# Kernel optimization log

Hardware: AMD Instinct MI355X
Metric: run time of the kernel (lower is better)

## Reference

```python
import jax, jax.numpy as jnp
import numpy as np

N_TYPES = 4
AEV_DIM = 384
HIDDEN = [160, 128, 96]
CELU_ALPHA = 0.1


def _init_params(key):
    dims = [AEV_DIM] + HIDDEN + [1]
    params = {}
    for li in range(len(dims) - 1):
        key, kw = jax.random.split(key)
        scale = 1.0 / np.sqrt(dims[li])
        # stacked over the N_TYPES per-atom-type experts
        params[f"W{li}"] = (jax.random.normal(kw, (N_TYPES, dims[li], dims[li + 1]), dtype=jnp.float32) * scale)
        params[f"b{li}"] = jnp.zeros((N_TYPES, dims[li + 1]), dtype=jnp.float32)
    return params


def setup_inputs() -> dict:
    key = jax.random.key(0)
    k1, k2, k3 = jax.random.split(key, 3)
    B, A = 2048, 64
    species = jax.random.randint(k1, (B, A), 0, N_TYPES, dtype=jnp.int64)
    aev = jax.random.normal(k2, (B, A, AEV_DIM), dtype=jnp.float32)
    inp = {"species": species, "aev": aev}
    inp.update(_init_params(k3))
    return inp


def _mlp(x, t, W0, b0, W1, b1, W2, b2, W3, b3):
    # x: [N, aev_dim] -> [N] per-atom energy for atom type t
    h = jax.nn.celu(x @ W0[t] + b0[t], alpha=CELU_ALPHA)
    h = jax.nn.celu(h @ W1[t] + b1[t], alpha=CELU_ALPHA)
    h = jax.nn.celu(h @ W2[t] + b2[t], alpha=CELU_ALPHA)
    return (h @ W3[t] + b3[t]).reshape(-1)


def reference(species, aev, W0, b0, W1, b1, W2, b2, W3, b3):
    B, A = species.shape
    sp = species.reshape(-1)            # [B*A]
    x = aev.reshape(-1, aev.shape[-1])  # [B*A, aev_dim]
    out = jnp.zeros(sp.shape, dtype=aev.dtype)  # padding_fill = 0
    for t in range(N_TYPES):  # fixed small expert set
        y = _mlp(x, t, W0, b0, W1, b1, W2, b2, W3, b3)
        out = jnp.where(sp == t, y, out)
    energies = out.reshape(B, A).sum(axis=1)  # reduce over atoms
    return species, energies
```

## Files before the change

### kernel.cpp

```cpp
#include <hip/hip_runtime.h>
#include <hip/hip_bf16.h>
#include <math.h>


#define NATOMS   131072
#define NMOL     2048
#define AEV      384
#define NTYPES   4
#define MBLK     64
#define PADTOT   (NATOMS + NTYPES * MBLK)
#define NBLK_MLP (PADTOT / MBLK)
#define NBLK_H   512

#define WB_L1 61440
#define WB_L2 81920
#define WB_T  94208

typedef __attribute__((ext_vector_type(8))) short bf16x8;
typedef __attribute__((ext_vector_type(4))) float f32x4;

__device__ __forceinline__ float celu01(float v) {
  return (v > 0.f) ? v : 0.1f * (__expf(v * 10.f) - 1.f);
}
__device__ __forceinline__ unsigned short f2bf(float x) {
  unsigned u = __float_as_uint(x);
  return (unsigned short)((u + 0x7FFFu + ((u >> 16) & 1u)) >> 16);
}
__device__ __forceinline__ unsigned int pk2(float lo, float hi) {
  union { __hip_bfloat162 h; unsigned int u; } c;
  c.h = __float22bfloat162_rn(make_float2(lo, hi));
  return c.u;
}
__device__ __forceinline__ bf16x8 cvt8(const float4 r0, const float4 r1) {
  union { unsigned int u[4]; bf16x8 v; } c;
  c.u[0] = pk2(r0.x, r0.y);
  c.u[1] = pk2(r0.z, r0.w);
  c.u[2] = pk2(r1.x, r1.y);
  c.u[3] = pk2(r1.z, r1.w);
  return c.v;
}


__global__ void k_pre(const int* __restrict__ species, float* __restrict__ out,
                      int* __restrict__ perm, int* __restrict__ hist,
                      const float* __restrict__ W0, const float* __restrict__ W1,
                      const float* __restrict__ W2, unsigned short* __restrict__ WB) {
  const int tid = threadIdx.x, blk = blockIdx.x;
  const int i = blk * 256 + tid;
  perm[i] = -1;
  if (i < NATOMS) out[i] = (float)species[i];
  if (i < NMOL) out[NATOMS + i] = 0.f;

  for (int f = i; f < NTYPES * WB_T; f += PADTOT) {
    const int t = f / WB_T, e0 = f - t * WB_T;
    int base, NT, N;
    const float* W;
    if (e0 < WB_L1)      { base = 0;     NT = 10; N = 160; W = W0 + (size_t)t * AEV * 160; }
    else if (e0 < WB_L2) { base = WB_L1; NT = 8;  N = 128; W = W1 + (size_t)t * 160 * 128; }
    else                 { base = WB_L2; NT = 6;  N = 96;  W = W2 + (size_t)t * 128 * 96; }
    const int e = e0 - base, frag = e >> 9, r = e & 511, lane = r >> 3, j = r & 7;
    const int kt = frag / NT, nt = frag - kt * NT;
    const int k = kt * 32 + ((lane >> 4) << 3) + j, n = nt * 16 + (lane & 15);
    WB[(size_t)t * WB_T + e0] = f2bf(W[k * N + n]);
  }

  if (blk < NBLK_H) {
    const int sp = species[i];
    const int wv = tid >> 6;
    __shared__ int wc[4 * NTYPES];
#pragma unroll
    for (int t = 0; t < NTYPES; ++t) {
      const unsigned long long m = __ballot(sp == t);
      if ((tid & 63) == 0) wc[wv * NTYPES + t] = __popcll(m);
    }
    __syncthreads();
    if (tid < NTYPES)
      hist[tid * NBLK_H + blk] = wc[tid] + wc[4 + tid] + wc[8 + tid] + wc[12 + tid];
  }
}


__global__ void k_scan(const int* __restrict__ hist, int* __restrict__ poff,
                       int* __restrict__ boff) {
  __shared__ int tot[NTYPES], base[NTYPES];
  const int tid = threadIdx.x, wv = tid >> 6, lane = tid & 63;
  int s = 0;
  for (int c = 0; c < 8; ++c) s += hist[wv * NBLK_H + c * 64 + lane];
  for (int off = 32; off; off >>= 1) s += __shfl_down(s, off);
  if (lane == 0) tot[wv] = s;
  __syncthreads();
  if (tid == 0) {
    int acc = 0; poff[0] = 0;
    for (int t = 0; t < NTYPES; ++t) {
      base[t] = acc;
      acc += ((tot[t] + 63) >> 6) << 6;
      poff[t + 1] = acc;
    }
  }
  __syncthreads();
  int carry = base[wv];
  for (int c = 0; c < 8; ++c) {
    const int orig = hist[wv * NBLK_H + c * 64 + lane];
    int v = orig;
    for (int off = 1; off < 64; off <<= 1) {
      const int u = __shfl_up(v, off);
      if (lane >= off) v += u;
    }
    boff[wv * NBLK_H + c * 64 + lane] = carry + v - orig;
    carry += __shfl(v, 63);
  }
}

__global__ void k_scatter(const int* __restrict__ species, const int* __restrict__ boff,
                          int* __restrict__ perm) {
  const int tid = threadIdx.x, blk = blockIdx.x;
  const int i = blk * 256 + tid;
  const int sp = species[i];
  const int wv = tid >> 6;
  __shared__ int wc[4 * NTYPES];
  unsigned long long msel = 0;
#pragma unroll
  for (int t = 0; t < NTYPES; ++t) {
    const unsigned long long m = __ballot(sp == t);
    if ((tid & 63) == 0) wc[wv * NTYPES + t] = __popcll(m);
    if (sp == t) msel = m;
  }
  __syncthreads();
  int woff = 0;
  for (int w = 0; w < wv; ++w) woff += wc[w * NTYPES + sp];
  const int rk = __builtin_amdgcn_mbcnt_hi((unsigned)(msel >> 32),
                 __builtin_amdgcn_mbcnt_lo((unsigned)msel, 0));
  perm[boff[sp * NBLK_H + blk] + woff + rk] = i;
}


__global__ __launch_bounds__(128, 2) void k_mlp(
    const float* __restrict__ aev, const unsigned short* __restrict__ WB,
    const float* __restrict__ b0, const float* __restrict__ b1,
    const float* __restrict__ b2, const float* __restrict__ b3,
    const float* __restrict__ W3,
    const int* __restrict__ poff, const int* __restrict__ perm,
    float* __restrict__ outE)
{
  __shared__ __align__(16) unsigned short H[64 * 168];
  __shared__ int permS[64];

  const int tid  = threadIdx.x;
  const int lane = tid & 63;
  const int wv   = __builtin_amdgcn_readfirstlane(tid >> 6);
  const int quad = lane >> 4, l15 = lane & 15;
  const int slot0 = blockIdx.x * MBLK;

  if (tid < 64) permS[tid] = perm[slot0 + tid];
  int t_ = (slot0 >= poff[1]) + (slot0 >= poff[2]) + (slot0 >= poff[3]);
  if (t_ > 3) t_ = 3;
  const int t = __builtin_amdgcn_readfirstlane(t_);
  __syncthreads();

  const float* rp[2];
#pragma unroll
  for (int mtl = 0; mtl < 2; ++mtl) {
    const int ai = permS[(2 * wv + mtl) * 16 + l15];
    rp[mtl] = aev + (size_t)(ai < 0 ? 0 : ai) * AEV + quad * 8;
  }

  const bf16x8* wb0 = (const bf16x8*)(WB + (size_t)t * WB_T);
  const bf16x8* wb1 = (const bf16x8*)(WB + (size_t)t * WB_T + WB_L1);
  const bf16x8* wb2 = (const bf16x8*)(WB + (size_t)t * WB_T + WB_L2);

  f32x4 acc0[10][2];
#pragma unroll
  for (int nt = 0; nt < 10; ++nt) {
    const float b = b0[t * 160 + nt * 16 + l15];
#pragma unroll
    for (int mtl = 0; mtl < 2; ++mtl) acc0[nt][mtl] = (f32x4){b, b, b, b};
  }

  bf16x8 wA[10], wB[10];
  float4 rA[2][2], rB[2][2];
#pragma unroll
  for (int nt = 0; nt < 10; ++nt) wA[nt] = wb0[nt * 64 + lane];
#pragma unroll
  for (int m = 0; m < 2; ++m) {
    rA[m][0] = *(const float4*)(rp[m]);
    rA[m][1] = *(const float4*)(rp[m] + 4);
    rB[m][0] = *(const float4*)(rp[m] + 32);
    rB[m][1] = *(const float4*)(rp[m] + 36);
  }

#define L0_STEP(KS, WC, WN, RC, PFW, PFR)                                      \
  {                                                                            \
    const bf16x8 a0 = cvt8(RC[0][0], RC[0][1]);                                \
    const bf16x8 a1 = cvt8(RC[1][0], RC[1][1]);                                \
    if (PFR) {                                                                 \
      _Pragma("unroll")                                                        \
      for (int m = 0; m < 2; ++m) {                                            \
        const float* p = rp[m] + (KS + 2) * 32;                                \
        RC[m][0] = *(const float4*)p;                                          \
        RC[m][1] = *(const float4*)(p + 4);                                    \
      }                                                                        \
    }                                                                          \
    if (PFW) {                                                                 \
      _Pragma("unroll")                                                        \
      for (int nt = 0; nt < 10; ++nt)                                          \
        WN[nt] = wb0[((KS + 1) * 10 + nt) * 64 + lane];                        \
    }                                                                          \
    _Pragma("unroll")                                                          \
    for (int nt = 0; nt < 10; ++nt) {                                          \
      acc0[nt][0] = __builtin_amdgcn_mfma_f32_16x16x32_bf16(a0, WC[nt], acc0[nt][0], 0, 0, 0); \
      acc0[nt][1] = __builtin_amdgcn_mfma_f32_16x16x32_bf16(a1, WC[nt], acc0[nt][1], 0, 0, 0); \
    }                                                                          \
  }

  L0_STEP(0,  wA, wB, rA, 1, 1)
  L0_STEP(1,  wB, wA, rB, 1, 1)
  L0_STEP(2,  wA, wB, rA, 1, 1)
  L0_STEP(3,  wB, wA, rB, 1, 1)
  L0_STEP(4,  wA, wB, rA, 1, 1)
  L0_STEP(5,  wB, wA, rB, 1, 1)
  L0_STEP(6,  wA, wB, rA, 1, 1)
  L0_STEP(7,  wB, wA, rB, 1, 1)
  L0_STEP(8,  wA, wB, rA, 1, 1)
  L0_STEP(9,  wB, wA, rB, 1, 1)
  L0_STEP(10, wA, wB, rA, 1, 0)
  L0_STEP(11, wB, wA, rB, 0, 0)
#undef L0_STEP

#pragma unroll
  for (int nt = 0; nt < 10; ++nt)
#pragma unroll
    for (int mtl = 0; mtl < 2; ++mtl)
#pragma unroll
      for (int r = 0; r < 4; ++r)
        H[((2 * wv + mtl) * 16 + quad * 4 + r) * 168 + nt * 16 + l15] = f2bf(celu01(acc0[nt][mtl][r]));
  __syncthreads();

  f32x4 acc1[8][2];
#pragma unroll
  for (int nt = 0; nt < 8; ++nt) {
    const float b = b1[t * 128 + nt * 16 + l15];
#pragma unroll
    for (int mtl = 0; mtl < 2; ++mtl) acc1[nt][mtl] = (f32x4){b, b, b, b};
  }
  bf16x8 w1A[8], w1B[8];
#pragma unroll
  for (int nt = 0; nt < 8; ++nt) w1A[nt] = wb1[nt * 64 + lane];

#define L1_STEP(KS, WC, WN, PFW)                                               \
  {                                                                            \
    const bf16x8 a0 = *(const bf16x8*)&H[((2 * wv + 0) * 16 + l15) * 168 + quad * 8 + (KS) * 32]; \
    const bf16x8 a1 = *(const bf16x8*)&H[((2 * wv + 1) * 16 + l15) * 168 + quad * 8 + (KS) * 32]; \
    if (PFW) {                                                                 \
      _Pragma("unroll")                                                        \
      for (int nt = 0; nt < 8; ++nt)                                           \
        WN[nt] = wb1[((KS + 1) * 8 + nt) * 64 + lane];                         \
    }                                                                          \
    _Pragma("unroll")                                                          \
    for (int nt = 0; nt < 8; ++nt) {                                           \
      acc1[nt][0] = __builtin_amdgcn_mfma_f32_16x16x32_bf16(a0, WC[nt], acc1[nt][0], 0, 0, 0); \
      acc1[nt][1] = __builtin_amdgcn_mfma_f32_16x16x32_bf16(a1, WC[nt], acc1[nt][1], 0, 0, 0); \
    }                                                                          \
  }

  L1_STEP(0, w1A, w1B, 1)
  L1_STEP(1, w1B, w1A, 1)
  L1_STEP(2, w1A, w1B, 1)
  L1_STEP(3, w1B, w1A, 1)
  L1_STEP(4, w1A, w1B, 0)
#undef L1_STEP

  __syncthreads();
#pragma unroll
  for (int nt = 0; nt < 8; ++nt)
#pragma unroll
    for (int mtl = 0; mtl < 2; ++mtl)
#pragma unroll
      for (int r = 0; r < 4; ++r)
        H[((2 * wv + mtl) * 16 + quad * 4 + r) * 136 + nt * 16 + l15] = f2bf(celu01(acc1[nt][mtl][r]));
  __syncthreads();

  f32x4 acc2[6][2];
#pragma unroll
  for (int nt = 0; nt < 6; ++nt) {
    const float b = b2[t * 96 + nt * 16 + l15];
#pragma unroll
    for (int mtl = 0; mtl < 2; ++mtl) acc2[nt][mtl] = (f32x4){b, b, b, b};
  }
  bf16x8 w2A[6], w2B[6];
#pragma unroll
  for (int nt = 0; nt < 6; ++nt) w2A[nt] = wb2[nt * 64 + lane];

#define L2_STEP(KS, WC, WN, PFW)                                               \
  {                                                                            \
    const bf16x8 a0 = *(const bf16x8*)&H[((2 * wv + 0) * 16 + l15) * 136 + quad * 8 + (KS) * 32]; \
    const bf16x8 a1 = *(const bf16x8*)&H[((2 * wv + 1) * 16 + l15) * 136 + quad * 8 + (KS) * 32]; \
    if (PFW) {                                                                 \
      _Pragma("unroll")                                                        \
      for (int nt = 0; nt < 6; ++nt)                                           \
        WN[nt] = wb2[((KS + 1) * 6 + nt) * 64 + lane];                         \
    }                                                                          \
    _Pragma("unroll")                                                          \
    for (int nt = 0; nt < 6; ++nt) {                                           \
      acc2[nt][0] = __builtin_amdgcn_mfma_f32_16x16x32_bf16(a0, WC[nt], acc2[nt][0], 0, 0, 0); \
      acc2[nt][1] = __builtin_amdgcn_mfma_f32_16x16x32_bf16(a1, WC[nt], acc2[nt][1], 0, 0, 0); \
    }                                                                          \
  }

  L2_STEP(0, w2A, w2B, 1)
  L2_STEP(1, w2B, w2A, 1)
  L2_STEP(2, w2A, w2B, 1)
  L2_STEP(3, w2B, w2A, 0)
#undef L2_STEP

  __syncthreads();
#pragma unroll
  for (int nt = 0; nt < 6; ++nt)
#pragma unroll
    for (int mtl = 0; mtl < 2; ++mtl)
#pragma unroll
      for (int r = 0; r < 4; ++r)
        H[((2 * wv + mtl) * 16 + quad * 4 + r) * 104 + nt * 16 + l15] = f2bf(celu01(acc2[nt][mtl][r]));
  __syncthreads();

  bf16x8 w3f[3];
#pragma unroll
  for (int ks = 0; ks < 3; ++ks) {
    const float* wp = W3 + t * 96 + ks * 32 + quad * 8;
    const float4 f0 = *(const float4*)wp;
    const float4 f1 = *(const float4*)(wp + 4);
    w3f[ks] = cvt8(f0, f1);
  }
  f32x4 accE[2];
#pragma unroll
  for (int mtl = 0; mtl < 2; ++mtl) accE[mtl] = (f32x4){0.f, 0.f, 0.f, 0.f};
#pragma unroll
  for (int mtl = 0; mtl < 2; ++mtl)
#pragma unroll
    for (int ks = 0; ks < 3; ++ks) {
      const bf16x8 a = *(const bf16x8*)&H[((2 * wv + mtl) * 16 + l15) * 104 + quad * 8 + ks * 32];
      accE[mtl] = __builtin_amdgcn_mfma_f32_16x16x32_bf16(a, w3f[ks], accE[mtl], 0, 0, 0);
    }
  const float bb3 = b3[t];
#pragma unroll
  for (int mtl = 0; mtl < 2; ++mtl)
#pragma unroll
    for (int r = 0; r < 4; ++r)
      if (l15 == 0) {
        const int ai = permS[(2 * wv + mtl) * 16 + quad * 4 + r];
        if (ai >= 0) atomicAdd(&outE[ai >> 6], accE[mtl][r] + bb3);
      }
}


extern "C" void kernel_launch(void* const* d_in, const int* in_sizes, int n_in,
                              void* d_out, int out_size, void* d_ws, size_t ws_size,
                              hipStream_t stream)
{
  const int*   species = (const int*)d_in[0];
  const float* aev     = (const float*)d_in[1];
  const float* W0 = (const float*)d_in[2];
  const float* b0 = (const float*)d_in[3];
  const float* W1 = (const float*)d_in[4];
  const float* b1 = (const float*)d_in[5];
  const float* W2 = (const float*)d_in[6];
  const float* b2 = (const float*)d_in[7];
  const float* W3 = (const float*)d_in[8];
  const float* b3 = (const float*)d_in[9];
  float* out = (float*)d_out;

  int* poff = (int*)d_ws;
  int* hist = poff + 8;
  int* boff = hist + NTYPES * NBLK_H;
  int* perm = boff + NTYPES * NBLK_H;
  unsigned short* WB = (unsigned short*)(perm + PADTOT);

  k_pre    <<<PADTOT / 256, 256, 0, stream>>>(species, out, perm, hist, W0, W1, W2, WB);
  k_scan   <<<1, 256, 0, stream>>>(hist, poff, boff);
  k_scatter<<<NBLK_H, 256, 0, stream>>>(species, boff, perm);
  k_mlp    <<<NBLK_MLP, 128, 0, stream>>>(aev, WB, b0, b1, b2, b3, W3,
                                          poff, perm, out + NATOMS);
}
```

Before: 401.7 us.

## Fuse scan into scatter, hand-roll bf16 packing, reorder weight prefetch with sched barriers

Merges the single-block scan kernel into the scatter kernel: each block recomputes the per-type totals and its own prefix from the histogram, which removes one launch and the boff buffer. The bf16 pair conversion now uses integer round-to-nearest-even in place of the HIP intrinsic. In all three MLP layers the next-step weight prefetch is issued before the activation loads and conversion, with a scheduling barrier to keep that order. The MLP kernel's launch bounds drop from 2 to 1 blocks per SM, which lets the compiler use more registers but may lower occupancy. The redundant histogram reads in every scatter block add some cost.

```diff
diff --git a/kernel.cpp b/kernel.cpp
--- a/kernel.cpp
+++ b/kernel.cpp
@@ -1,5 +1,4 @@
 #include <hip/hip_runtime.h>
-#include <hip/hip_bf16.h>
 #include <math.h>
 
 
@@ -27,9 +26,10 @@
   return (unsigned short)((u + 0x7FFFu + ((u >> 16) & 1u)) >> 16);
 }
 __device__ __forceinline__ unsigned int pk2(float lo, float hi) {
-  union { __hip_bfloat162 h; unsigned int u; } c;
-  c.h = __float22bfloat162_rn(make_float2(lo, hi));
-  return c.u;
+  unsigned a = __float_as_uint(lo), b = __float_as_uint(hi);
+  a = (a + 0x7FFFu + ((a >> 16) & 1u)) >> 16;
+  b = ((b + 0x7FFFu + ((b >> 16) & 1u)) >> 16) << 16;
+  return a | b;
 }
 __device__ __forceinline__ bf16x8 cvt8(const float4 r0, const float4 r1) {
   union { unsigned int u[4]; bf16x8 v; } c;
@@ -80,43 +80,38 @@
 }
 
 
-__global__ void k_scan(const int* __restrict__ hist, int* __restrict__ poff,
-                       int* __restrict__ boff) {
-  __shared__ int tot[NTYPES], base[NTYPES];
-  const int tid = threadIdx.x, wv = tid >> 6, lane = tid & 63;
-  int s = 0;
-  for (int c = 0; c < 8; ++c) s += hist[wv * NBLK_H + c * 64 + lane];
-  for (int off = 32; off; off >>= 1) s += __shfl_down(s, off);
-  if (lane == 0) tot[wv] = s;
+__global__ void k_sct(const int* __restrict__ species, const int* __restrict__ hist,
+                      int* __restrict__ poff, int* __restrict__ perm) {
+  __shared__ int tot[NTYPES], preS[NTYPES], bofS[NTYPES];
+  const int tid = threadIdx.x, blk = blockIdx.x;
+  const int wv = tid >> 6, lane = tid & 63;
+
+  int s = 0, p = 0;
+  for (int c = 0; c < 8; ++c) {
+    const int idx = c * 64 + lane;
+    const int h = hist[wv * NBLK_H + idx];
+    s += h;
+    if (idx < blk) p += h;
+  }
+  for (int off = 32; off; off >>= 1) {
+    s += __shfl_down(s, off);
+    p += __shfl_down(p, off);
+  }
+  if (lane == 0) { tot[wv] = s; preS[wv] = p; }
   __syncthreads();
   if (tid == 0) {
-    int acc = 0; poff[0] = 0;
+    int acc = 0;
     for (int t = 0; t < NTYPES; ++t) {
-      base[t] = acc;
+      bofS[t] = acc + preS[t];
       acc += ((tot[t] + 63) >> 6) << 6;
-      poff[t + 1] = acc;
+      if (blk == 0) poff[t + 1] = acc;
     }
-  }
-  __syncthreads();
-  int carry = base[wv];
-  for (int c = 0; c < 8; ++c) {
-    const int orig = hist[wv * NBLK_H + c * 64 + lane];
-    int v = orig;
-    for (int off = 1; off < 64; off <<= 1) {
-      const int u = __shfl_up(v, off);
-      if (lane >= off) v += u;
-    }
-    boff[wv * NBLK_H + c * 64 + lane] = carry + v - orig;
-    carry += __shfl(v, 63);
-  }
-}
-
-__global__ void k_scatter(const int* __restrict__ species, const int* __restrict__ boff,
-                          int* __restrict__ perm) {
-  const int tid = threadIdx.x, blk = blockIdx.x;
+    if (blk == 0) poff[0] = 0;
+  }
+  __syncthreads();
+
   const int i = blk * 256 + tid;
   const int sp = species[i];
-  const int wv = tid >> 6;
   __shared__ int wc[4 * NTYPES];
   unsigned long long msel = 0;
 #pragma unroll
@@ -130,11 +125,11 @@
   for (int w = 0; w < wv; ++w) woff += wc[w * NTYPES + sp];
   const int rk = __builtin_amdgcn_mbcnt_hi((unsigned)(msel >> 32),
                  __builtin_amdgcn_mbcnt_lo((unsigned)msel, 0));
-  perm[boff[sp * NBLK_H + blk] + woff + rk] = i;
-}
-
-
-__global__ __launch_bounds__(128, 2) void k_mlp(
+  perm[bofS[sp] + woff + rk] = i;
+}
+
+
+__global__ __launch_bounds__(128, 1) void k_mlp(
     const float* __restrict__ aev, const unsigned short* __restrict__ WB,
     const float* __restrict__ b0, const float* __restrict__ b1,
     const float* __restrict__ b2, const float* __restrict__ b3,
@@ -190,6 +185,12 @@
 
 #define L0_STEP(KS, WC, WN, RC, PFW, PFR)                                      \
   {                                                                            \
+    if (PFW) {                                                                 \
+      _Pragma("unroll")                                                        \
+      for (int nt = 0; nt < 10; ++nt)                                          \
+        WN[nt] = wb0[((KS + 1) * 10 + nt) * 64 + lane];                        \
+    }                                                                          \
+    __builtin_amdgcn_sched_barrier(0);                                         \
     const bf16x8 a0 = cvt8(RC[0][0], RC[0][1]);                                \
     const bf16x8 a1 = cvt8(RC[1][0], RC[1][1]);                                \
     if (PFR) {                                                                 \
@@ -199,11 +200,6 @@
         RC[m][0] = *(const float4*)p;                                          \
         RC[m][1] = *(const float4*)(p + 4);                                    \
       }                                                                        \
-    }                                                                          \
-    if (PFW) {                                                                 \
-      _Pragma("unroll")                                                        \
-      for (int nt = 0; nt < 10; ++nt)                                          \
-        WN[nt] = wb0[((KS + 1) * 10 + nt) * 64 + lane];                        \
     }                                                                          \
     _Pragma("unroll")                                                          \
     for (int nt = 0; nt < 10; ++nt) {                                          \
@@ -248,13 +244,14 @@
 
 #define L1_STEP(KS, WC, WN, PFW)                                               \
   {                                                                            \
-    const bf16x8 a0 = *(const bf16x8*)&H[((2 * wv + 0) * 16 + l15) * 168 + quad * 8 + (KS) * 32]; \
-    const bf16x8 a1 = *(const bf16x8*)&H[((2 * wv + 1) * 16 + l15) * 168 + quad * 8 + (KS) * 32]; \
     if (PFW) {                                                                 \
       _Pragma("unroll")                                                        \
       for (int nt = 0; nt < 8; ++nt)                                           \
         WN[nt] = wb1[((KS + 1) * 8 + nt) * 64 + lane];                         \
     }                                                                          \
+    __builtin_amdgcn_sched_barrier(0);                                         \
+    const bf16x8 a0 = *(const bf16x8*)&H[((2 * wv + 0) * 16 + l15) * 168 + quad * 8 + (KS) * 32]; \
+    const bf16x8 a1 = *(const bf16x8*)&H[((2 * wv + 1) * 16 + l15) * 168 + quad * 8 + (KS) * 32]; \
     _Pragma("unroll")                                                          \
     for (int nt = 0; nt < 8; ++nt) {                                           \
       acc1[nt][0] = __builtin_amdgcn_mfma_f32_16x16x32_bf16(a0, WC[nt], acc1[nt][0], 0, 0, 0); \
@@ -292,13 +289,14 @@
 
 #define L2_STEP(KS, WC, WN, PFW)                                               \
   {                                                                            \
-    const bf16x8 a0 = *(const bf16x8*)&H[((2 * wv + 0) * 16 + l15) * 136 + quad * 8 + (KS) * 32]; \
-    const bf16x8 a1 = *(const bf16x8*)&H[((2 * wv + 1) * 16 + l15) * 136 + quad * 8 + (KS) * 32]; \
     if (PFW) {                                                                 \
       _Pragma("unroll")                                                        \
       for (int nt = 0; nt < 6; ++nt)                                           \
         WN[nt] = wb2[((KS + 1) * 6 + nt) * 64 + lane];                         \
     }                                                                          \
+    __builtin_amdgcn_sched_barrier(0);                                         \
+    const bf16x8 a0 = *(const bf16x8*)&H[((2 * wv + 0) * 16 + l15) * 136 + quad * 8 + (KS) * 32]; \
+    const bf16x8 a1 = *(const bf16x8*)&H[((2 * wv + 1) * 16 + l15) * 136 + quad * 8 + (KS) * 32]; \
     _Pragma("unroll")                                                          \
     for (int nt = 0; nt < 6; ++nt) {                                           \
       acc2[nt][0] = __builtin_amdgcn_mfma_f32_16x16x32_bf16(a0, WC[nt], acc2[nt][0], 0, 0, 0); \
@@ -370,13 +368,11 @@
 
   int* poff = (int*)d_ws;
   int* hist = poff + 8;
-  int* boff = hist + NTYPES * NBLK_H;
-  int* perm = boff + NTYPES * NBLK_H;
+  int* perm = hist + NTYPES * NBLK_H;
   unsigned short* WB = (unsigned short*)(perm + PADTOT);
 
-  k_pre    <<<PADTOT / 256, 256, 0, stream>>>(species, out, perm, hist, W0, W1, W2, WB);
-  k_scan   <<<1, 256, 0, stream>>>(hist, poff, boff);
-  k_scatter<<<NBLK_H, 256, 0, stream>>>(species, boff, perm);
-  k_mlp    <<<NBLK_MLP, 128, 0, stream>>>(aev, WB, b0, b1, b2, b3, W3,
-                                          poff, perm, out + NATOMS);
-}
+  k_pre<<<PADTOT / 256, 256, 0, stream>>>(species, out, perm, hist, W0, W1, W2, WB);
+  k_sct<<<NBLK_H, 256, 0, stream>>>(species, hist, poff, perm);
+  k_mlp<<<NBLK_MLP, 128, 0, stream>>>(aev, WB, b0, b1, b2, b3, W3,
+                                      poff, perm, out + NATOMS);
+}
```

After: 340.7 us. 15.2% less time.
